# Kernel tuning notes

Hardware: AMD Instinct MI355X
Metric: run time of the kernel (lower is better)

Reference implementation:

```python
import math
import jax, jax.numpy as jnp
import numpy as np

B, CH, PN, PS = 8, 19, 128, 200
RES, SKIP, NB, S4C = 256, 256, 6, 4
L = CH * PN            # 2432, flattened (channel, patch) length
H2 = 2 * RES           # 512, S4 / attention width


def _conv1d(x, w, b, pad):
    y = jax.lax.conv_general_dilated(x, w, (1,), [(pad, pad)], dimension_numbers=('NCH', 'OIH', 'NCH'))
    return y + b[None, :, None]


def _conv2d(x, w, b, stride, pad, groups=1):
    y = jax.lax.conv_general_dilated(x, w, stride, pad, dimension_numbers=('NCHW', 'OIHW', 'NCHW'), feature_group_count=groups)
    return y + b[None, :, None, None]


def _gn(x, w, b, groups=5, eps=1e-5):
    b_, c, hh, ww = x.shape
    xg = x.reshape(b_, groups, c // groups, hh, ww)
    m = xg.mean((2, 3, 4), keepdims=True)
    v = xg.var((2, 3, 4), keepdims=True)
    xg = (xg - m) / jnp.sqrt(v + eps)
    return xg.reshape(b_, c, hh, ww) * w[None, :, None, None] + b[None, :, None, None]


def _rms(x, scale, eps=1e-8):
    # RMSNorm over channel dim (dim=1), matching source exactly
    rms = jnp.linalg.norm(x, axis=1, keepdims=True) / jnp.sqrt(jnp.asarray(x.shape[1], x.dtype))
    return scale[None, :, None] * x / (rms + eps)


def _gelu(x):
    return jax.nn.gelu(x, approximate=False)


def _forward(x, pe_w, pe_b, pi0_w, pi0_b, gn0_w, gn0_b, pi1_w, pi1_b, gn1_w, gn1_b, pi2_w, pi2_b, gn2_w, gn2_b, spec_w, spec_b, ic_w, ic_b, blk_sn, blk_cw, blk_cb, blk_k, blk_D, blk_ow, blk_ob, blk_Wv, blk_bv, blk_Wo, blk_bo, blk_rw, blk_rb, blk_sw, blk_sb, fc_w, fc_b, zc_w, zc_b, ln_w, ln_b):
    # ---------------- PatchEmbedding ----------------
    mx = x.reshape(B, 1, CH * PN, PS)
    p = _conv2d(mx, pi0_w, pi0_b, (1, 25), [(0, 0), (24, 24)])          # (B,25,CH*PN,8)
    p = _gelu(_gn(p, gn0_w, gn0_b))
    p = _gelu(_gn(_conv2d(p, pi1_w, pi1_b, (1, 1), [(0, 0), (1, 1)]), gn1_w, gn1_b))
    p = _gelu(_gn(_conv2d(p, pi2_w, pi2_b, (1, 1), [(0, 0), (1, 1)]), gn2_w, gn2_b))
    pe = jnp.transpose(p, (0, 2, 1, 3)).reshape(B, CH, PN, PS)
    spec = jnp.abs(jnp.fft.rfft(x, norm='forward'))                       # (B,CH,PN,101)
    pe = pe + jnp.einsum('bcnf,pf->bcnp', spec, spec_w) + spec_b
    pos = _conv2d(jnp.transpose(pe, (0, 3, 1, 2)), pe_w, pe_b, (1, 1), [(9, 9), (3, 3)], groups=PS)
    pe = pe + jnp.transpose(pos, (0, 2, 3, 1))
    # ---------------- b c s p -> b p (c s) ----------------
    h = jnp.transpose(pe, (0, 3, 1, 2)).reshape(B, PS, L)
    noise = jax.nn.relu(_conv1d(h, ic_w, ic_b, 0))                        # (B,RES,L)
    # ---------------- Residual group ----------------
    sk = jnp.zeros((B, SKIP, L), noise.dtype)
    hx = noise
    for i in range(NB):
        hn = _rms(hx, blk_sn[i])
        u = _gelu(_conv1d(hx + noise, blk_cw[i], blk_cb[i], 1))           # (B,H2,L)
        # S4 GConv: FFT long convolution + D skip + GLU output linear
        n = 2 * L
        uf = jnp.fft.rfft(u, n=n)                                          # (B,H2,n/2+1)
        kf = jnp.fft.rfft(blk_k[i], n=n)                                   # (S4C,H2,n/2+1)
        y = jnp.fft.irfft(uf[:, None] * kf[None], n=n)[..., :L]           # (B,S4C,H2,L)
        y = y + u[:, None] * blk_D[i][None, :, :, None]
        y = y.reshape(B, S4C * H2, L)
        y = jnp.einsum('bcl,oc->bol', y, blk_ow[i]) + blk_ob[i][None, :, None]
        h_t = y[:, :H2] * jax.nn.sigmoid(y[:, H2:])                        # GLU -> (B,H2,L)
        # window_size=1 local attention degenerates to out_proj(v_proj(x))
        v = jnp.einsum('bcl,vc->bvl', h_t, blk_Wv[i]) + blk_bv[i][None, :, None]
        a = jnp.einsum('bvl,ov->bol', v, blk_Wo[i]) + blk_bo[i][None, :, None]
        g = h_t + a
        out = jnp.tanh(g[:, :RES]) * jax.nn.sigmoid(g[:, RES:])
        hx = (hn + _conv1d(out, blk_rw[i], blk_rb[i], 0)) * math.sqrt(0.5)
        sk = sk + _conv1d(out, blk_sw[i], blk_sb[i], 0)
    sk = sk * math.sqrt(1.0 / NB)
    # ---------------- final conv + norm ----------------
    o = jax.nn.relu(_conv1d(sk, fc_w, fc_b, 0))
    o = _conv1d(o, zc_w, zc_b, 0)                                          # (B,PS,L)
    o = jnp.transpose(o.reshape(B, PS, CH, PN), (0, 2, 3, 1))              # (B,CH,PN,PS)
    m = o.mean(-1, keepdims=True)
    var = o.var(-1, keepdims=True)
    return (o - m) / jnp.sqrt(var + 1e-5) * ln_w + ln_b


def setup_inputs():
    key = jax.random.key(0)
    keys = iter(jax.random.split(key, 40))
    def rn(shape, s=0.02):
        return jax.random.normal(next(keys), shape, jnp.float32) * s
    d = {}
    d['x'] = jax.random.normal(next(keys), (B, CH, PN, PS), jnp.float32)
    d['pe_w'] = rn((PS, 1, 19, 7)); d['pe_b'] = jnp.zeros((PS,), jnp.float32)
    d['pi0_w'] = rn((25, 1, 1, 49)); d['pi0_b'] = jnp.zeros((25,), jnp.float32)
    d['gn0_w'] = jnp.ones((25,), jnp.float32); d['gn0_b'] = jnp.zeros((25,), jnp.float32)
    d['pi1_w'] = rn((25, 25, 1, 3)); d['pi1_b'] = jnp.zeros((25,), jnp.float32)
    d['gn1_w'] = jnp.ones((25,), jnp.float32); d['gn1_b'] = jnp.zeros((25,), jnp.float32)
    d['pi2_w'] = rn((25, 25, 1, 3)); d['pi2_b'] = jnp.zeros((25,), jnp.float32)
    d['gn2_w'] = jnp.ones((25,), jnp.float32); d['gn2_b'] = jnp.zeros((25,), jnp.float32)
    d['spec_w'] = rn((PS, 101)); d['spec_b'] = jnp.zeros((PS,), jnp.float32)
    d['ic_w'] = rn((RES, PS, 1)); d['ic_b'] = jnp.zeros((RES,), jnp.float32)
    d['blk_sn'] = jnp.ones((NB, RES), jnp.float32)
    d['blk_cw'] = rn((NB, H2, RES, 3)); d['blk_cb'] = jnp.zeros((NB, H2), jnp.float32)
    d['blk_k'] = rn((NB, S4C, H2, L), 0.005); d['blk_D'] = rn((NB, S4C, H2), 0.1)
    d['blk_ow'] = rn((NB, 2 * H2, S4C * H2)); d['blk_ob'] = jnp.zeros((NB, 2 * H2), jnp.float32)
    d['blk_Wv'] = rn((NB, H2, H2)); d['blk_bv'] = jnp.zeros((NB, H2), jnp.float32)
    d['blk_Wo'] = rn((NB, H2, H2)); d['blk_bo'] = jnp.zeros((NB, H2), jnp.float32)
    d['blk_rw'] = rn((NB, RES, RES, 1)); d['blk_rb'] = jnp.zeros((NB, RES), jnp.float32)
    d['blk_sw'] = rn((NB, SKIP, RES, 1)); d['blk_sb'] = jnp.zeros((NB, SKIP), jnp.float32)
    d['fc_w'] = rn((SKIP, SKIP, 1)); d['fc_b'] = jnp.zeros((SKIP,), jnp.float32)
    d['zc_w'] = rn((PS, SKIP, 1)); d['zc_b'] = jnp.zeros((PS,), jnp.float32)
    d['ln_w'] = jnp.ones((PS,), jnp.float32); d['ln_b'] = jnp.zeros((PS,), jnp.float32)
    return d


def reference(x, pe_w, pe_b, pi0_w, pi0_b, gn0_w, gn0_b, pi1_w, pi1_b, gn1_w, gn1_b, pi2_w, pi2_b, gn2_w, gn2_b, spec_w, spec_b, ic_w, ic_b, blk_sn, blk_cw, blk_cb, blk_k, blk_D, blk_ow, blk_ob, blk_Wv, blk_bv, blk_Wo, blk_bo, blk_rw, blk_rb, blk_sw, blk_sb, fc_w, fc_b, zc_w, zc_b, ln_w, ln_b):
    return _forward(x, pe_w, pe_b, pi0_w, pi0_b, gn0_w, gn0_b, pi1_w, pi1_b, gn1_w, gn1_b, pi2_w, pi2_b, gn2_w, gn2_b, spec_w, spec_b, ic_w, ic_b, blk_sn, blk_cw, blk_cb, blk_k, blk_D, blk_ow, blk_ob, blk_Wv, blk_bv, blk_Wo, blk_bo, blk_rw, blk_rb, blk_sw, blk_sb, fc_w, fc_b, zc_w, zc_b, ln_w, ln_b)
```

## Files before the change

kernel.cpp:

```cpp
#include <hip/hip_runtime.h>
#include <hip/hip_bf16.h>
#include <math.h>

#define LSEQ 2432

typedef short bf16x8 __attribute__((ext_vector_type(8)));
typedef float f32x4 __attribute__((ext_vector_type(4)));
typedef unsigned int u32;

__device__ __forceinline__ float gelu_f(float x){
  return 0.5f * x * (1.0f + erff(x * 0.70710678118654752440f));
}
__device__ __forceinline__ float sigmoid_f(float x){
  return 1.0f / (1.0f + __expf(-x));
}
__device__ __forceinline__ unsigned short f2bf(float f){
  __hip_bfloat16 h = __float2bfloat16(f);
  return *reinterpret_cast<unsigned short*>(&h);
}
__device__ __forceinline__ float bfu2f(unsigned short s){
  union { u32 u; float f; } X; X.u = ((u32)s) << 16; return X.f;
}
__device__ __forceinline__ u32 packsplit(float v){
  unsigned short hi = f2bf(v);
  float lo = v - bfu2f(hi);
  unsigned short ls = f2bf(lo);
  return (u32)hi | ((u32)ls << 16);
}

__global__ __launch_bounds__(256) void k_pi0(const float* __restrict__ x,
    const float* __restrict__ w, const float* __restrict__ bias,
    float* __restrict__ out){
  int idx = blockIdx.x * 256 + threadIdx.x;
  int o = blockIdx.y, b = blockIdx.z;
  int r = idx >> 3, wv = idx & 7;
  const float* xr = x + ((size_t)b * 2432 + r) * 200;
  const float* wt = w + o * 49;
  float acc = bias[o];
  int start = wv * 25 - 24;
  #pragma unroll
  for (int t = 0; t < 49; ++t){
    int ix = start + t;
    if (ix >= 0 && ix < 200) acc += xr[ix] * wt[t];
  }
  out[(((size_t)b * 25 + o) * 2432 + r) * 8 + wv] = acc;
}

__global__ __launch_bounds__(256) void k_gn_reduce(const float* __restrict__ p, float* __restrict__ stats){
  int b = blockIdx.x / 5, g = blockIdx.x % 5;
  const float* base = p + ((size_t)b * 25 + g * 5) * 19456;
  float s = 0.f, s2 = 0.f;
  for (int i = threadIdx.x; i < 97280; i += 256){ float v = base[i]; s += v; s2 += v * v; }
  __shared__ float sh[256], sh2[256];
  int t = threadIdx.x;
  sh[t] = s; sh2[t] = s2; __syncthreads();
  for (int off = 128; off > 0; off >>= 1){
    if (t < off){ sh[t] += sh[t+off]; sh2[t] += sh2[t+off]; }
    __syncthreads();
  }
  if (t == 0){
    float m = sh[0] / 97280.f;
    float var = sh2[0] / 97280.f - m * m;
    stats[blockIdx.x * 2] = m;
    stats[blockIdx.x * 2 + 1] = rsqrtf(var + 1e-5f);
  }
}

__global__ __launch_bounds__(256) void k_gn_apply(float* __restrict__ p, const float* __restrict__ stats,
    const float* __restrict__ gw, const float* __restrict__ gb){
  size_t i = (size_t)blockIdx.x * 256 + threadIdx.x;
  int c = (int)((i / 19456) % 25);
  int b = (int)(i / 486400);
  int g = c / 5;
  float m = stats[(b*5+g)*2], istd = stats[(b*5+g)*2+1];
  float v = (p[i] - m) * istd * gw[c] + gb[c];
  p[i] = gelu_f(v);
}

__global__ __launch_bounds__(256) void k_pconv3(const float* __restrict__ pin,
    const float* __restrict__ w, const float* __restrict__ bias, float* __restrict__ pout){
  int idx = blockIdx.x * 256 + threadIdx.x;
  int o = blockIdx.y, b = blockIdx.z;
  int r = idx >> 3, wv = idx & 7;
  const float* ib = pin + (size_t)b * 25 * 19456 + r * 8 + wv;
  const float* wo = w + o * 75;
  float acc = bias[o];
  #pragma unroll
  for (int i = 0; i < 25; ++i){
    const float* row = ib + (size_t)i * 19456;
    float w0 = wo[i*3], w1 = wo[i*3+1], w2 = wo[i*3+2];
    if (wv > 0) acc += row[-1] * w0;
    acc += row[0] * w1;
    if (wv < 7) acc += row[1] * w2;
  }
  pout[(((size_t)b*25 + o) * 2432 + r) * 8 + wv] = acc;
}

__global__ __launch_bounds__(256) void k_pe_build(const float* __restrict__ p2, float* __restrict__ pe){
  size_t i = (size_t)blockIdx.x * 256 + threadIdx.x;
  int p = (int)(i % 200);
  size_t rem = i / 200;
  int l = (int)(rem % 2432);
  int b = (int)(rem / 2432);
  pe[i] = p2[(((size_t)b*25 + (p>>3)) * 2432 + l) * 8 + (p & 7)];
}

__global__ __launch_bounds__(256) void k_spec(const float* __restrict__ x, float* __restrict__ spec){
  __shared__ float xr[200], ct[200], st[200];
  int row = blockIdx.x;
  int t = threadIdx.x;
  if (t < 200){
    xr[t] = x[(size_t)row * 200 + t];
    float ang = -0.031415926535897932385f * t;
    ct[t] = cosf(ang); st[t] = sinf(ang);
  }
  __syncthreads();
  if (t < 101){
    float re = 0.f, im = 0.f;
    int ph = 0;
    for (int k = 0; k < 200; ++k){
      re += xr[k] * ct[ph];
      im += xr[k] * st[ph];
      ph += t; if (ph >= 200) ph -= 200;
    }
    spec[(size_t)row * 101 + t] = sqrtf(re*re + im*im) * 0.005f;
  }
}

__global__ __launch_bounds__(256) void k_spec_mm(const float* __restrict__ spec,
    const float* __restrict__ sw, const float* __restrict__ sb, float* __restrict__ pe){
  __shared__ float sr[101];
  int row = blockIdx.x;
  int t = threadIdx.x;
  if (t < 101) sr[t] = spec[(size_t)row * 101 + t];
  __syncthreads();
  if (t < 200){
    const float* wr = sw + t * 101;
    float acc = sb[t];
    for (int f = 0; f < 101; ++f) acc += sr[f] * wr[f];
    pe[(size_t)row * 200 + t] += acc;
  }
}

__global__ __launch_bounds__(256) void k_trp(const float* __restrict__ pe, float* __restrict__ peT){
  __shared__ float ts[32][33];
  int l0 = blockIdx.x * 32, c0 = blockIdx.y * 32, b = blockIdx.z;
  int t = threadIdx.x;
  int i = t >> 5, j = t & 31;
  #pragma unroll
  for (int pass = 0; pass < 4; ++pass){
    int ii = i + pass * 8;
    int c = c0 + j;
    ts[ii][j] = (c < 200) ? pe[((size_t)b * 2432 + l0 + ii) * 200 + c] : 0.f;
  }
  __syncthreads();
  #pragma unroll
  for (int pass = 0; pass < 4; ++pass){
    int ii = i + pass * 8;
    int c = c0 + ii;
    if (c < 200) peT[((size_t)b * 200 + c) * 2432 + l0 + j] = ts[j][ii];
  }
}

__global__ __launch_bounds__(128) void k_hbuild2(const float* __restrict__ peT,
    const float* __restrict__ pw, const float* __restrict__ pb, float* __restrict__ h){
  __shared__ float T[19][136];
  __shared__ float wsh[133];
  int c = blockIdx.x, p = blockIdx.y, b = blockIdx.z;
  int tid = threadIdx.x;
  const float* pr = peT + ((size_t)b * 200 + p) * 2432;
  for (int e = tid; e < 19 * 136; e += 128){
    int a = e / 136, m = e % 136;
    int hh = c - 9 + a, ww = m - 3;
    float v = 0.f;
    if (hh >= 0 && hh < 19 && ww >= 0 && ww < 128) v = pr[hh * 128 + ww];
    T[a][m] = v;
  }
  for (int e = tid; e < 133; e += 128) wsh[e] = pw[p * 133 + e];
  __syncthreads();
  int j = tid;
  float conv = pb[p];
  #pragma unroll
  for (int a = 0; a < 19; ++a){
    #pragma unroll
    for (int tt = 0; tt < 7; ++tt) conv += T[a][j + tt] * wsh[a * 7 + tt];
  }
  float orig = T[9][j + 3];
  h[((size_t)b * 200 + p) * 2432 + c * 128 + j] = orig + conv;
}

__global__ __launch_bounds__(256) void k_wcast(const float* __restrict__ src,
    unsigned short* __restrict__ dst, int O, int Kin, int Kpad){
  size_t i = (size_t)blockIdx.x * 256 + threadIdx.x;
  if (i >= (size_t)O * Kpad) return;
  int k = (int)(i % Kpad);
  int o = (int)(i / Kpad);
  dst[i] = (k < Kin) ? f2bf(src[(size_t)o * Kin + k]) : 0;
}

__global__ __launch_bounds__(256) void k_wcast_glu(const float* __restrict__ src,
    unsigned short* __restrict__ dst){
  size_t i = (size_t)blockIdx.x * 256 + threadIdx.x;
  if (i >= (size_t)6 * 1024 * 2048) return;
  int k = (int)(i % 2048);
  size_t rem = i / 2048;
  int ro = (int)(rem % 1024);
  int blk = (int)(rem / 1024);
  int j = (ro >> 1) + (ro & 1) * 512;
  dst[i] = f2bf(src[((size_t)blk * 1024 + j) * 2048 + k]);
}

__global__ __launch_bounds__(256) void k_castT(const float* __restrict__ in,
    unsigned short* __restrict__ out, int C, int Kpad, int cbase){
  __shared__ float ts[32][33];
  int l0 = blockIdx.x * 32, c0 = blockIdx.y * 32, b = blockIdx.z;
  int t = threadIdx.x;
  int i = t >> 5, j = t & 31;
  #pragma unroll
  for (int pass = 0; pass < 4; ++pass){
    int ci = c0 + i + pass * 8;
    ts[i + pass * 8][j] = (ci < C) ? in[((size_t)b * C + ci) * LSEQ + l0 + j] : 0.f;
  }
  __syncthreads();
  #pragma unroll
  for (int pass = 0; pass < 4; ++pass){
    int li = l0 + i + pass * 8;
    out[((size_t)b * LSEQ + li) * Kpad + cbase + c0 + j] = f2bf(ts[j][i + pass * 8]);
  }
}

__global__ __launch_bounds__(256) void k_packT(const float* __restrict__ A,
    const float* __restrict__ N, u32* __restrict__ out){
  __shared__ float ts[32][33];
  int l0 = blockIdx.x * 32, c0 = blockIdx.y * 32, b = blockIdx.z;
  int t = threadIdx.x;
  int i = t >> 5, j = t & 31;
  #pragma unroll
  for (int pass = 0; pass < 4; ++pass){
    int ci = c0 + i + pass * 8;
    size_t ii = ((size_t)b * 256 + ci) * LSEQ + l0 + j;
    ts[i + pass * 8][j] = A[ii] + N[ii];
  }
  __syncthreads();
  #pragma unroll
  for (int pass = 0; pass < 4; ++pass){
    int li = l0 + i + pass * 8;
    out[((size_t)b * LSEQ + li) * 256 + c0 + j] = packsplit(ts[j][i + pass * 8]);
  }
}

__global__ __launch_bounds__(256) void k_wpack3(const float* __restrict__ cw, u32* __restrict__ Wp){
  int i = blockIdx.x * 256 + threadIdx.x;
  int o = i / 768, rem = i % 768;
  int t = rem / 256, c = rem % 256;
  Wp[i] = packsplit(cw[((size_t)o * 256 + c) * 3 + t]);
}

__global__ __launch_bounds__(256) void k_gateT(const float* __restrict__ ht,
    const float* __restrict__ a, unsigned short* __restrict__ out){
  __shared__ float ts[32][33];
  int l0 = blockIdx.x * 32, c0 = blockIdx.y * 32, b = blockIdx.z;
  int t = threadIdx.x;
  int i = t >> 5, j = t & 31;
  #pragma unroll
  for (int pass = 0; pass < 4; ++pass){
    int ci = c0 + i + pass * 8;
    size_t i1 = ((size_t)b * 512 + ci) * LSEQ + l0 + j;
    size_t i2 = ((size_t)b * 512 + ci + 256) * LSEQ + l0 + j;
    float g1 = ht[i1] + a[i1];
    float g2 = ht[i2] + a[i2];
    ts[i + pass * 8][j] = tanhf(g1) * sigmoid_f(g2);
  }
  __syncthreads();
  #pragma unroll
  for (int pass = 0; pass < 4; ++pass){
    int li = l0 + i + pass * 8;
    out[((size_t)b * LSEQ + li) * 256 + c0 + j] = f2bf(ts[j][i + pass * 8]);
  }
}

__global__ __launch_bounds__(256) void k_rmsr(const float* __restrict__ hx, float* __restrict__ rinv){
  int idx = blockIdx.x * 256 + threadIdx.x;
  int b = idx / 2432, l = idx % 2432;
  const float* p = hx + (size_t)b * 256 * LSEQ + l;
  float s = 0.f;
  #pragma unroll 8
  for (int c = 0; c < 256; ++c){ float v = p[(size_t)c * LSEQ]; s += v * v; }
  rinv[idx] = 1.0f / (sqrtf(s * (1.0f/256.0f)) + 1e-8f);
}

__global__ __launch_bounds__(256) void k_bgemm(const unsigned short* __restrict__ Wb,
    const unsigned short* __restrict__ Xb, const float* __restrict__ bias,
    const float* __restrict__ res, const float* __restrict__ sn,
    const float* __restrict__ rinv, float* __restrict__ out,
    int O, int Kpad, float alpha, float fs, int act, int accf){
  __shared__ unsigned short Ws[128 * 40];
  __shared__ unsigned short Xs[128 * 40];
  int l0 = blockIdx.x * 128, o0 = blockIdx.y * 128, b = blockIdx.z;
  int tid = threadIdx.x;
  int w = tid >> 6, lane = tid & 63;
  int ow_ = (w & 1) * 64, lw_ = (w >> 1) * 64;
  int m = lane & 15, q = (lane >> 4) & 3;
  const unsigned short* Xbb = Xb + (size_t)b * 2432 * Kpad;
  f32x4 acc[4][4] = {};
  for (int k0 = 0; k0 < Kpad; k0 += 32){
    #pragma unroll
    for (int r = 0; r < 2; ++r){
      int idx = tid + r * 256;
      int row = idx >> 2, cq = (idx & 3) * 8;
      uint4 v = make_uint4(0u, 0u, 0u, 0u);
      int o = o0 + row;
      if (o < O) v = *(const uint4*)(Wb + (size_t)o * Kpad + k0 + cq);
      *(uint4*)&Ws[row * 40 + cq] = v;
      uint4 xv = *(const uint4*)(Xbb + (size_t)(l0 + row) * Kpad + k0 + cq);
      *(uint4*)&Xs[row * 40 + cq] = xv;
    }
    __syncthreads();
    bf16x8 A[4], Bf[4];
    #pragma unroll
    for (int t = 0; t < 4; ++t) A[t] = *(const bf16x8*)&Ws[(ow_ + t * 16 + m) * 40 + q * 8];
    #pragma unroll
    for (int u = 0; u < 4; ++u) Bf[u] = *(const bf16x8*)&Xs[(lw_ + u * 16 + m) * 40 + q * 8];
    #pragma unroll
    for (int t = 0; t < 4; ++t)
      #pragma unroll
      for (int u = 0; u < 4; ++u)
        acc[t][u] = __builtin_amdgcn_mfma_f32_16x16x32_bf16(A[t], Bf[u], acc[t][u], 0, 0, 0);
    __syncthreads();
  }
  if (act == 3){
    #pragma unroll
    for (int t = 0; t < 4; ++t){
      #pragma unroll
      for (int u = 0; u < 4; ++u){
        int l = l0 + lw_ + u * 16 + m;
        #pragma unroll
        for (int r = 0; r < 4; r += 2){
          int ro = o0 + ow_ + t * 16 + q * 4 + r;
          int j = ro >> 1;
          float v1 = acc[t][u][r]   + bias[j];
          float v2 = acc[t][u][r+1] + bias[j + 512];
          out[((size_t)b * 512 + j) * LSEQ + l] = v1 * sigmoid_f(v2);
        }
      }
    }
    return;
  }
  #pragma unroll
  for (int t = 0; t < 4; ++t){
    #pragma unroll
    for (int u = 0; u < 4; ++u){
      int l = l0 + lw_ + u * 16 + m;
      #pragma unroll
      for (int r = 0; r < 4; ++r){
        int o = o0 + ow_ + t * 16 + q * 4 + r;
        if (o >= O) continue;
        size_t oi = ((size_t)b * O + o) * LSEQ + l;
        float v = alpha * acc[t][u][r];
        if (bias) v += bias[o];
        if (res){
          if (sn) v += sn[o] * res[oi] * rinv[b * 2432 + l];
          else v += res[oi];
        }
        if (accf) v += out[oi];
        if (act == 1) v = fmaxf(v, 0.f);
        out[oi] = v * fs;
      }
    }
  }
}

__device__ __forceinline__ bf16x8 s4_mk(u32 a, u32 b, u32 c, u32 d){
  union { u32 u[4]; bf16x8 v; } X; X.u[0]=a; X.u[1]=b; X.u[2]=c; X.u[3]=d; return X.v;
}
#define S4_P16H(a,b) __builtin_amdgcn_perm((a),(b),0x05040100u)
#define S4_P16L(a,b) __builtin_amdgcn_perm((a),(b),0x07060302u)

__global__ __launch_bounds__(256) void k_conv3m(const u32* __restrict__ Wp,
    const float* __restrict__ bias, const u32* __restrict__ Xp, float* __restrict__ U){
  __shared__ u32 Ws[128 * 36];
  __shared__ u32 Xs[128 * 36];
  int l0 = blockIdx.x * 128, o0 = blockIdx.y * 128, b = blockIdx.z;
  int tid = threadIdx.x;
  int w = tid >> 6, lane = tid & 63;
  int ow_ = (w & 1) * 64, lw_ = (w >> 1) * 64;
  int m = lane & 15, q = (lane >> 4) & 3;
  const u32* Xb = Xp + (size_t)b * 2432 * 256;
  f32x4 acc[4][4] = {};
  for (int s = 0; s < 24; ++s){
    int t = s >> 3, k0 = (s & 7) << 5;
    #pragma unroll
    for (int r = 0; r < 4; ++r){
      int idx = tid + r * 256;
      int row = idx >> 3, cq = (idx & 7) * 4;
      *(uint4*)&Ws[row * 36 + cq] = *(const uint4*)(Wp + (size_t)(o0 + row) * 768 + t * 256 + k0 + cq);
      int li = l0 + row + t - 1;
      uint4 xv = make_uint4(0u, 0u, 0u, 0u);
      if (li >= 0 && li < 2432) xv = *(const uint4*)(Xb + (size_t)li * 256 + k0 + cq);
      *(uint4*)&Xs[row * 36 + cq] = xv;
    }
    __syncthreads();
    bf16x8 Ah[4], Al[4], Bh[4], Bl[4];
    #pragma unroll
    for (int tt = 0; tt < 4; ++tt){
      const u32* p = &Ws[(ow_ + tt * 16 + m) * 36 + q * 8];
      u32 w0=p[0],w1=p[1],w2=p[2],w3=p[3],w4=p[4],w5=p[5],w6=p[6],w7=p[7];
      Ah[tt] = s4_mk(S4_P16H(w1,w0), S4_P16H(w3,w2), S4_P16H(w5,w4), S4_P16H(w7,w6));
      Al[tt] = s4_mk(S4_P16L(w1,w0), S4_P16L(w3,w2), S4_P16L(w5,w4), S4_P16L(w7,w6));
    }
    #pragma unroll
    for (int uu = 0; uu < 4; ++uu){
      const u32* p = &Xs[(lw_ + uu * 16 + m) * 36 + q * 8];
      u32 w0=p[0],w1=p[1],w2=p[2],w3=p[3],w4=p[4],w5=p[5],w6=p[6],w7=p[7];
      Bh[uu] = s4_mk(S4_P16H(w1,w0), S4_P16H(w3,w2), S4_P16H(w5,w4), S4_P16H(w7,w6));
      Bl[uu] = s4_mk(S4_P16L(w1,w0), S4_P16L(w3,w2), S4_P16L(w5,w4), S4_P16L(w7,w6));
    }
    #pragma unroll
    for (int tt = 0; tt < 4; ++tt)
      #pragma unroll
      for (int uu = 0; uu < 4; ++uu){
        acc[tt][uu] = __builtin_amdgcn_mfma_f32_16x16x32_bf16(Ah[tt], Bh[uu], acc[tt][uu], 0, 0, 0);
        acc[tt][uu] = __builtin_amdgcn_mfma_f32_16x16x32_bf16(Al[tt], Bh[uu], acc[tt][uu], 0, 0, 0);
        acc[tt][uu] = __builtin_amdgcn_mfma_f32_16x16x32_bf16(Ah[tt], Bl[uu], acc[tt][uu], 0, 0, 0);
      }
    __syncthreads();
  }
  #pragma unroll
  for (int tt = 0; tt < 4; ++tt){
    #pragma unroll
    for (int uu = 0; uu < 4; ++uu){
      int l = l0 + lw_ + uu * 16 + m;
      #pragma unroll
      for (int r = 0; r < 4; ++r){
        int o = o0 + ow_ + tt * 16 + q * 4 + r;
        U[((size_t)b * 512 + o) * LSEQ + l] = gelu_f(acc[tt][uu][r] + bias[o]);
      }
    }
  }
}

#define S4_SU 2464
#define S4_UPLANE (8*S4_SU*2)
#define S4_ULO  S4_UPLANE
#define S4_REV  (2*S4_UPLANE)
#define S4_TS   (S4_REV + 2856*4)
#define S4_LDSZ (S4_TS + 4*576)

#define S4_FILL(SL) { \
  int Wc = Wp > 0 ? Wp : 0; \
  int ib = rl + Wc; \
  u32 w0=RV[ib], w1=RV[ib+1], w2=RV[ib+2], w3=RV[ib+3], w4=RV[ib+4], w5=RV[ib+5], w6=RV[ib+6], w7=RV[ib+7]; \
  Ph[SL] = s4_mk(S4_P16H(w1,w0), S4_P16H(w3,w2), S4_P16H(w5,w4), S4_P16H(w7,w6)); \
  Pl[SL] = s4_mk(S4_P16L(w1,w0), S4_P16L(w3,w2), S4_P16L(w5,w4), S4_P16L(w7,w6)); \
  Wp -= 32; }

#define S4_MM(ph,d,BH,BL) \
  acc[d] = __builtin_amdgcn_mfma_f32_16x16x32_bf16(Ph[((ph)+5+(d))%12], BH, acc[d], 0, 0, 0); \
  acc[d] = __builtin_amdgcn_mfma_f32_16x16x32_bf16(Pl[((ph)+5+(d))%12], BH, acc[d], 0, 0, 0); \
  acc[d] = __builtin_amdgcn_mfma_f32_16x16x32_bf16(Ph[((ph)+5+(d))%12], BL, acc[d], 0, 0, 0);

#define S4_PHASE(ph,BC,BN) { \
  S4_FILL(((ph)+4)%12); \
  int bn = j0 - 32; bn = bn > 2400 ? 2400 : bn; bn = bn < 0 ? 2432 : bn; \
  const char* bp = LB + ubo + 2*bn; \
  Bh##BN = *(const bf16x8*)bp; \
  Bl##BN = *(const bf16x8*)(bp + S4_ULO); \
  S4_MM(ph,0,Bh##BC,Bl##BC) S4_MM(ph,1,Bh##BC,Bl##BC) S4_MM(ph,2,Bh##BC,Bl##BC) S4_MM(ph,3,Bh##BC,Bl##BC) \
  S4_MM(ph,4,Bh##BC,Bl##BC) S4_MM(ph,5,Bh##BC,Bl##BC) S4_MM(ph,6,Bh##BC,Bl##BC) S4_MM(ph,7,Bh##BC,Bl##BC) \
  j0 -= 32; }

__global__ __launch_bounds__(256, 1) void k_s4m(const float* __restrict__ ksrc,
    const float* __restrict__ Dv, const float* __restrict__ u, float* __restrict__ y){
  extern __shared__ char LB[];
  ushort* UH = (ushort*)LB;
  ushort* UL = (ushort*)(LB + S4_ULO);
  u32* RV = (u32*)(LB + S4_REV);
  int h = blockIdx.x;
  int tid = threadIdx.x;
  for (int e = tid; e < 8 * 608; e += 256){
    int b = e / 608, c4 = e % 608;
    float4 v = *(const float4*)(u + ((size_t)b * 512 + h) * 2432 + c4 * 4);
    u32 p0 = packsplit(v.x), p1 = packsplit(v.y), p2 = packsplit(v.z), p3 = packsplit(v.w);
    uint2 hw, lw;
    hw.x = (p0 & 0xffffu) | (p1 << 16);
    hw.y = (p2 & 0xffffu) | (p3 << 16);
    lw.x = (p0 >> 16) | (p1 & 0xffff0000u);
    lw.y = (p2 >> 16) | (p3 & 0xffff0000u);
    *(uint2*)(LB + (size_t)b * (S4_SU*2) + c4 * 8) = hw;
    *(uint2*)(LB + S4_ULO + (size_t)b * (S4_SU*2) + c4 * 8) = lw;
  }
  if (tid < 256){
    int b = tid >> 5, i = tid & 31;
    UH[b * S4_SU + 2432 + i] = 0;
    UL[b * S4_SU + 2432 + i] = 0;
  }
  {
    const float* kg = ksrc + (size_t)h * 2432;
    for (int e = tid; e < 2856; e += 256){
      u32 v = 0;
      int t = 2704 - e;
      if (t >= 0 && t < 2432) v = packsplit(kg[t]);
      RV[e] = v;
    }
  }
  __syncthreads();

  int lane = tid & 63;
  int wid = __builtin_amdgcn_readfirstlane(tid >> 6);
  int m = lane & 15, qq = lane >> 4;
  int rl = 16 - m + 8 * qq;
  int ubo = (m & 7) * (S4_SU*2) + qq * 16;
  float dv = Dv[h];
  float* TSp = (float*)(LB + S4_TS + wid * 576);
  static const int GT[2][5] = {{9,6,4,2,0},{8,7,5,3,1}};

  #pragma unroll 1
  for (int c = 0; c < 5; ++c){
    int g = GT[wid >> 1][c];
    int Lb = 256 * g + ((wid & 1) << 4);
    int ltop = Lb + 224;
    int J0 = ((ltop + 15) >> 5) << 5;
    int W0 = 2688 - ltop + J0;
    int NS = (J0 >> 5) + 1;
    int nIt = (NS + 11) / 12;

    f32x4 acc[8];
    bf16x8 Ph[12], Pl[12];
    bf16x8 Bh0, Bl0, Bh1, Bl1;
    {
      f32x4 za = {0.f, 0.f, 0.f, 0.f};
      acc[0]=za; acc[1]=za; acc[2]=za; acc[3]=za; acc[4]=za; acc[5]=za; acc[6]=za; acc[7]=za;
      bf16x8 zz = s4_mk(0u,0u,0u,0u);
      Ph[5]=zz; Ph[6]=zz; Ph[7]=zz; Ph[8]=zz; Ph[9]=zz; Ph[10]=zz; Ph[11]=zz; Ph[4]=zz;
      Pl[5]=zz; Pl[6]=zz; Pl[7]=zz; Pl[8]=zz; Pl[9]=zz; Pl[10]=zz; Pl[11]=zz; Pl[4]=zz;
    }
    int Wp = W0;
    S4_FILL(0) S4_FILL(1) S4_FILL(2) S4_FILL(3)
    int j0 = J0;
    {
      int bj0 = j0 > 2400 ? 2400 : j0;
      const char* bp0 = LB + ubo + 2 * bj0;
      Bh0 = *(const bf16x8*)bp0;
      Bl0 = *(const bf16x8*)(bp0 + S4_ULO);
    }
    #pragma unroll 1
    for (int it = 0; it < nIt; ++it){
      S4_PHASE(0,0,1) S4_PHASE(1,1,0) S4_PHASE(2,0,1) S4_PHASE(3,1,0)
      S4_PHASE(4,0,1) S4_PHASE(5,1,0) S4_PHASE(6,0,1) S4_PHASE(7,1,0)
      S4_PHASE(8,0,1) S4_PHASE(9,1,0) S4_PHASE(10,0,1) S4_PHASE(11,1,0)
    }
    #pragma unroll
    for (int d = 0; d < 8; ++d){
      int ld = Lb + 32 * d;
      if (ld < 2432){
        if (m < 8){
          TSp[(qq*4+0)*9 + m] = acc[d][0];
          TSp[(qq*4+1)*9 + m] = acc[d][1];
          TSp[(qq*4+2)*9 + m] = acc[d][2];
          TSp[(qq*4+3)*9 + m] = acc[d][3];
        }
        __builtin_amdgcn_wave_barrier();
        #pragma unroll
        for (int p = 0; p < 2; ++p){
          int li = lane & 15, bb = (lane >> 4) + 4 * p;
          float v = TSp[li*9 + bb];
          int l = ld + li;
          float uv = bfu2f(UH[bb * S4_SU + l]) + bfu2f(UL[bb * S4_SU + l]);
          y[((size_t)bb * 512 + h) * 2432 + l] = v + dv * uv;
        }
        __builtin_amdgcn_wave_barrier();
      }
    }
  }
}

__global__ __launch_bounds__(256) void k_ln(const float* __restrict__ o2,
    const float* __restrict__ lw, const float* __restrict__ lb2, float* __restrict__ out){
  __shared__ float s1[256], s2[256];
  int row = blockIdx.x;
  int b = row / 2432, l = row % 2432;
  int t = threadIdx.x;
  float v = 0.f;
  if (t < 200) v = o2[((size_t)b * 200 + t) * LSEQ + l];
  s1[t] = v; s2[t] = v * v;
  __syncthreads();
  for (int off = 128; off > 0; off >>= 1){
    if (t < off){ s1[t] += s1[t + off]; s2[t] += s2[t + off]; }
    __syncthreads();
  }
  float m = s1[0] * 0.005f;
  float var = s2[0] * 0.005f - m * m;
  float istd = rsqrtf(var + 1e-5f);
  if (t < 200) out[(size_t)row * 200 + t] = (v - m) * istd * lw[t] + lb2[t];
}

extern "C" void kernel_launch(void* const* d_in, const int* in_sizes, int n_in,
                              void* d_out, int out_size, void* d_ws, size_t ws_size,
                              hipStream_t stream){
  const float* x     = (const float*)d_in[0];
  const float* pe_w  = (const float*)d_in[1];
  const float* pe_b  = (const float*)d_in[2];
  const float* pi0_w = (const float*)d_in[3];
  const float* pi0_b = (const float*)d_in[4];
  const float* gn0_w = (const float*)d_in[5];
  const float* gn0_b = (const float*)d_in[6];
  const float* pi1_w = (const float*)d_in[7];
  const float* pi1_b = (const float*)d_in[8];
  const float* gn1_w = (const float*)d_in[9];
  const float* gn1_b = (const float*)d_in[10];
  const float* pi2_w = (const float*)d_in[11];
  const float* pi2_b = (const float*)d_in[12];
  const float* gn2_w = (const float*)d_in[13];
  const float* gn2_b = (const float*)d_in[14];
  const float* spec_w= (const float*)d_in[15];
  const float* spec_b= (const float*)d_in[16];
  const float* ic_w  = (const float*)d_in[17];
  const float* ic_b  = (const float*)d_in[18];
  const float* blk_sn= (const float*)d_in[19];
  const float* blk_cw= (const float*)d_in[20];
  const float* blk_cb= (const float*)d_in[21];
  const float* blk_k = (const float*)d_in[22];
  const float* blk_D = (const float*)d_in[23];
  const float* blk_ow= (const float*)d_in[24];
  const float* blk_ob= (const float*)d_in[25];
  const float* blk_Wv= (const float*)d_in[26];
  const float* blk_bv= (const float*)d_in[27];
  const float* blk_Wo= (const float*)d_in[28];
  const float* blk_bo= (const float*)d_in[29];
  const float* blk_rw= (const float*)d_in[30];
  const float* blk_rb= (const float*)d_in[31];
  const float* blk_sw= (const float*)d_in[32];
  const float* blk_sb= (const float*)d_in[33];
  const float* fc_w  = (const float*)d_in[34];
  const float* fc_b  = (const float*)d_in[35];
  const float* zc_w  = (const float*)d_in[36];
  const float* zc_b  = (const float*)d_in[37];
  const float* ln_w  = (const float*)d_in[38];
  const float* ln_b  = (const float*)d_in[39];

  static int s4m_attr = 0;
  if (!s4m_attr){
    hipFuncSetAttribute(reinterpret_cast<const void*>(k_s4m),
                        hipFuncAttributeMaxDynamicSharedMemorySize, S4_LDSZ);
    s4m_attr = 1;
  }

  float* Wsp = (float*)d_ws;
  const size_t NLL = (size_t)8 * 256 * 2432;
  float* noise = Wsp;
  float* hxb   = Wsp + NLL;
  float* skb   = Wsp + 2 * NLL;
  float* ub    = Wsp + 3 * NLL;
  float* ysb   = Wsp + 5 * NLL;
  float* htb   = ysb;
  unsigned short* actT = (unsigned short*)(Wsp + 7 * NLL);
  unsigned short* wB = (unsigned short*)(Wsp + 11 * NLL);
  unsigned short* owB = wB;
  unsigned short* WvB = wB + 12582912;
  unsigned short* WoB = wB + 14155776;
  unsigned short* rwB = wB + 15728640;
  unsigned short* swB = wB + 16121856;
  unsigned short* icB = wB + 16515072;
  unsigned short* fcB = wB + 16572416;
  unsigned short* zcB = wB + 16637952;
  float* rinv   = Wsp + 11 * NLL + 8344576;
  float* gnstats= rinv + 19456;
  u32* WpB = (u32*)(Wsp + 63152208);
  u32* XpT = (u32*)(Wsp + 7 * NLL);

  float* p0 = ub;
  float* p1 = ysb;
  float* p2 = ub;
  float* pe = Wsp + 7 * NLL;
  float* spec = Wsp + 8 * NLL;
  float* peT = skb;
  float* hb = hxb;

  const float SQ05 = 0.70710678118654752440f;
  const float SQ16 = 0.40824829046386301637f;

  k_wcast_glu<<<49152,256,0,stream>>>(blk_ow, owB);
  k_wcast<<<(3072*512+255)/256,256,0,stream>>>(blk_Wv, WvB, 3072, 512, 512);
  k_wcast<<<(3072*512+255)/256,256,0,stream>>>(blk_Wo, WoB, 3072, 512, 512);
  k_wcast<<<(1536*256+255)/256,256,0,stream>>>(blk_rw, rwB, 1536, 256, 256);
  k_wcast<<<(1536*256+255)/256,256,0,stream>>>(blk_sw, swB, 1536, 256, 256);
  k_wcast<<<(256*224+255)/256,256,0,stream>>>(ic_w, icB, 256, 200, 224);
  k_wcast<<<(256*256+255)/256,256,0,stream>>>(fc_w, fcB, 256, 256, 256);
  k_wcast<<<(200*256+255)/256,256,0,stream>>>(zc_w, zcB, 200, 256, 256);

  k_pi0<<<dim3(76,25,8), 256, 0, stream>>>(x, pi0_w, pi0_b, p0);
  k_gn_reduce<<<40,256,0,stream>>>(p0, gnstats);
  k_gn_apply<<<15200,256,0,stream>>>(p0, gnstats, gn0_w, gn0_b);
  k_pconv3<<<dim3(76,25,8),256,0,stream>>>(p0, pi1_w, pi1_b, p1);
  k_gn_reduce<<<40,256,0,stream>>>(p1, gnstats);
  k_gn_apply<<<15200,256,0,stream>>>(p1, gnstats, gn1_w, gn1_b);
  k_pconv3<<<dim3(76,25,8),256,0,stream>>>(p1, pi2_w, pi2_b, p2);
  k_gn_reduce<<<40,256,0,stream>>>(p2, gnstats);
  k_gn_apply<<<15200,256,0,stream>>>(p2, gnstats, gn2_w, gn2_b);
  k_pe_build<<<15200,256,0,stream>>>(p2, pe);
  k_spec<<<19456,256,0,stream>>>(x, spec);
  k_spec_mm<<<19456,256,0,stream>>>(spec, spec_w, spec_b, pe);
  k_trp<<<dim3(76,7,8),256,0,stream>>>(pe, peT);
  k_hbuild2<<<dim3(19,200,8),128,0,stream>>>(peT, pe_w, pe_b, hb);
  k_castT<<<dim3(76,7,8),256,0,stream>>>(hb, actT, 200, 224, 0);
  k_bgemm<<<dim3(19,2,8),256,0,stream>>>(icB, actT, ic_b, nullptr, nullptr, nullptr,
                                         noise, 256, 224, 1.f, 1.f, 1, 0);
  hipMemcpyAsync(hxb, noise, NLL * sizeof(float), hipMemcpyDeviceToDevice, stream);

  for (int i = 0; i < 6; ++i){
    const float* sn = blk_sn + i * 256;
    const float* cw = blk_cw + (size_t)i * 512 * 768;
    const float* cb = blk_cb + i * 512;
    const float* ob = blk_ob + i * 1024;
    const float* bv = blk_bv + i * 512;
    const float* bo = blk_bo + i * 512;
    const float* rb = blk_rb + i * 256;
    const float* sb = blk_sb + i * 256;

    k_rmsr<<<76,256,0,stream>>>(hxb, rinv);
    k_packT<<<dim3(76,8,8),256,0,stream>>>(hxb, noise, XpT);
    k_wpack3<<<1536,256,0,stream>>>(cw, WpB);
    k_conv3m<<<dim3(19,4,8),256,0,stream>>>(WpB, cb, XpT, ub);
    for (int s = 0; s < 4; ++s){
      const float* kw = blk_k + ((size_t)i * 4 + s) * 512 * 2432;
      const float* Dvp = blk_D + ((size_t)i * 4 + s) * 512;
      k_s4m<<<dim3(512),256,S4_LDSZ,stream>>>(kw, Dvp, ub, ysb);
      k_castT<<<dim3(76,16,8),256,0,stream>>>(ysb, actT, 512, 2048, s * 512);
    }
    k_bgemm<<<dim3(19,8,8),256,0,stream>>>(owB + (size_t)i*1024*2048, actT, ob,
                                           nullptr, nullptr, nullptr, htb,
                                           1024, 2048, 1.f, 1.f, 3, 0);
    k_castT<<<dim3(76,16,8),256,0,stream>>>(htb, actT, 512, 512, 0);
    k_bgemm<<<dim3(19,4,8),256,0,stream>>>(WvB + (size_t)i*512*512, actT, bv,
                                           nullptr, nullptr, nullptr, ub,
                                           512, 512, 1.f, 1.f, 0, 0);
    k_castT<<<dim3(76,16,8),256,0,stream>>>(ub, actT, 512, 512, 0);
    k_bgemm<<<dim3(19,4,8),256,0,stream>>>(WoB + (size_t)i*512*512, actT, bo,
                                           nullptr, nullptr, nullptr, ub,
                                           512, 512, 1.f, 1.f, 0, 0);
    k_gateT<<<dim3(76,8,8),256,0,stream>>>(htb, ub, actT);
    k_bgemm<<<dim3(19,2,8),256,0,stream>>>(rwB + (size_t)i*256*256, actT, rb,
                                           hxb, sn, rinv, hxb,
                                           256, 256, 1.f, SQ05, 0, 0);
    k_bgemm<<<dim3(19,2,8),256,0,stream>>>(swB + (size_t)i*256*256, actT, sb,
                                           nullptr, nullptr, nullptr, skb,
                                           256, 256, 1.f, 1.f, 0, i==0?0:1);
  }

  k_castT<<<dim3(76,8,8),256,0,stream>>>(skb, actT, 256, 256, 0);
  k_bgemm<<<dim3(19,2,8),256,0,stream>>>(fcB, actT, fc_b, nullptr, nullptr, nullptr,
                                         ub, 256, 256, SQ16, 1.f, 1, 0);
  k_castT<<<dim3(76,8,8),256,0,stream>>>(ub, actT, 256, 256, 0);
  k_bgemm<<<dim3(19,2,8),256,0,stream>>>(zcB, actT, zc_b, nullptr, nullptr, nullptr,
                                         ysb, 200, 256, 1.f, 1.f, 0, 0);
  k_ln<<<19456,256,0,stream>>>(ysb, ln_w, ln_b, (float*)d_out);
}
```

Baseline: 9.410 ms.

## Widen S4 kernel to 8 waves with rebalanced chunk schedule; tile patch convs in LDS

The S4 long-convolution kernel now runs 512 threads (8 waves) per head instead of 256. A new per-wave chunk table spreads the 20 causal half-chunks across waves to balance the triangular workload, and the per-wave scratch region in LDS grows to match. The patch-embedding conv kernels (pi0 and the 3-tap pconv) now stage input rows and weights in shared memory and compute all 25 output channels per thread, which removes redundant global reads across the output-channel grid dimension. Risks are more LDS and register pressure in k_s4m and higher register use in the conv kernels, which hold 49 or 75 values per thread.

```diff
diff --git a/kernel.cpp b/kernel.cpp
--- a/kernel.cpp
+++ b/kernel.cpp
@@ -28,22 +28,36 @@
   return (u32)hi | ((u32)ls << 16);
 }
 
-__global__ __launch_bounds__(256) void k_pi0(const float* __restrict__ x,
+__global__ __launch_bounds__(256) void k_pi0b(const float* __restrict__ x,
     const float* __restrict__ w, const float* __restrict__ bias,
     float* __restrict__ out){
-  int idx = blockIdx.x * 256 + threadIdx.x;
-  int o = blockIdx.y, b = blockIdx.z;
-  int r = idx >> 3, wv = idx & 7;
-  const float* xr = x + ((size_t)b * 2432 + r) * 200;
-  const float* wt = w + o * 49;
-  float acc = bias[o];
+  __shared__ float xs[32][200];
+  __shared__ float ws[25][49];
+  __shared__ float bs[25];
+  int r0 = blockIdx.x * 32, b = blockIdx.y;
+  int tid = threadIdx.x;
+  const float* xb = x + ((size_t)b * 2432 + r0) * 200;
+  for (int e = tid; e < 1600; e += 256){
+    int row = e / 50, c4 = e % 50;
+    *(float4*)&xs[row][c4 * 4] = *(const float4*)(xb + row * 200 + c4 * 4);
+  }
+  for (int e = tid; e < 1225; e += 256) ws[e / 49][e % 49] = w[e];
+  if (tid < 25) bs[tid] = bias[tid];
+  __syncthreads();
+  int row = tid >> 3, wv = tid & 7;
   int start = wv * 25 - 24;
+  float tap[49];
   #pragma unroll
   for (int t = 0; t < 49; ++t){
     int ix = start + t;
-    if (ix >= 0 && ix < 200) acc += xr[ix] * wt[t];
-  }
-  out[(((size_t)b * 25 + o) * 2432 + r) * 8 + wv] = acc;
+    tap[t] = (ix >= 0 && ix < 200) ? xs[row][ix] : 0.f;
+  }
+  for (int o = 0; o < 25; ++o){
+    float acc = bs[o];
+    #pragma unroll
+    for (int t = 0; t < 49; ++t) acc += tap[t] * ws[o][t];
+    out[(((size_t)b * 25 + o) * 2432 + (r0 + row)) * 8 + wv] = acc;
+  }
 }
 
 __global__ __launch_bounds__(256) void k_gn_reduce(const float* __restrict__ p, float* __restrict__ stats){
@@ -77,23 +91,36 @@
   p[i] = gelu_f(v);
 }
 
-__global__ __launch_bounds__(256) void k_pconv3(const float* __restrict__ pin,
+__global__ __launch_bounds__(256) void k_pconv3b(const float* __restrict__ pin,
     const float* __restrict__ w, const float* __restrict__ bias, float* __restrict__ pout){
-  int idx = blockIdx.x * 256 + threadIdx.x;
-  int o = blockIdx.y, b = blockIdx.z;
-  int r = idx >> 3, wv = idx & 7;
-  const float* ib = pin + (size_t)b * 25 * 19456 + r * 8 + wv;
-  const float* wo = w + o * 75;
-  float acc = bias[o];
+  __shared__ float T[25][256];
+  __shared__ float ws[25][75];
+  __shared__ float bs[25];
+  int r0 = blockIdx.x * 32, b = blockIdx.y;
+  int tid = threadIdx.x;
+  const float* pb = pin + (size_t)b * 25 * 19456 + r0 * 8;
+  for (int e = tid; e < 25 * 64; e += 256){
+    int i = e / 64, c4 = e % 64;
+    *(float4*)&T[i][c4 * 4] = *(const float4*)(pb + (size_t)i * 19456 + c4 * 4);
+  }
+  for (int e = tid; e < 1875; e += 256) ws[e / 75][e % 75] = w[e];
+  if (tid < 25) bs[tid] = bias[tid];
+  __syncthreads();
+  int wv = tid & 7;
+  float xm[25], x0[25], xp[25];
   #pragma unroll
   for (int i = 0; i < 25; ++i){
-    const float* row = ib + (size_t)i * 19456;
-    float w0 = wo[i*3], w1 = wo[i*3+1], w2 = wo[i*3+2];
-    if (wv > 0) acc += row[-1] * w0;
-    acc += row[0] * w1;
-    if (wv < 7) acc += row[1] * w2;
-  }
-  pout[(((size_t)b*25 + o) * 2432 + r) * 8 + wv] = acc;
+    x0[i] = T[i][tid];
+    xm[i] = (wv > 0) ? T[i][tid - 1] : 0.f;
+    xp[i] = (wv < 7) ? T[i][tid + 1] : 0.f;
+  }
+  for (int o = 0; o < 25; ++o){
+    float acc = bs[o];
+    #pragma unroll
+    for (int i = 0; i < 25; ++i)
+      acc += xm[i] * ws[o][i*3] + x0[i] * ws[o][i*3+1] + xp[i] * ws[o][i*3+2];
+    pout[(((size_t)b * 25 + o) * 2432 + r0) * 8 + tid] = acc;
+  }
 }
 
 __global__ __launch_bounds__(256) void k_pe_build(const float* __restrict__ p2, float* __restrict__ pe){
@@ -444,7 +471,7 @@
 #define S4_ULO  S4_UPLANE
 #define S4_REV  (2*S4_UPLANE)
 #define S4_TS   (S4_REV + 2856*4)
-#define S4_LDSZ (S4_TS + 4*576)
+#define S4_LDSZ (S4_TS + 8*576*4)
 
 #define S4_FILL(SL) { \
   int Wc = Wp > 0 ? Wp : 0; \
@@ -469,7 +496,7 @@
   S4_MM(ph,4,Bh##BC,Bl##BC) S4_MM(ph,5,Bh##BC,Bl##BC) S4_MM(ph,6,Bh##BC,Bl##BC) S4_MM(ph,7,Bh##BC,Bl##BC) \
   j0 -= 32; }
 
-__global__ __launch_bounds__(256, 1) void k_s4m(const float* __restrict__ ksrc,
+__global__ __launch_bounds__(512, 1) void k_s4m(const float* __restrict__ ksrc,
     const float* __restrict__ Dv, const float* __restrict__ u, float* __restrict__ y){
   extern __shared__ char LB[];
   ushort* UH = (ushort*)LB;
@@ -477,7 +504,7 @@
   u32* RV = (u32*)(LB + S4_REV);
   int h = blockIdx.x;
   int tid = threadIdx.x;
-  for (int e = tid; e < 8 * 608; e += 256){
+  for (int e = tid; e < 8 * 608; e += 512){
     int b = e / 608, c4 = e % 608;
     float4 v = *(const float4*)(u + ((size_t)b * 512 + h) * 2432 + c4 * 4);
     u32 p0 = packsplit(v.x), p1 = packsplit(v.y), p2 = packsplit(v.z), p3 = packsplit(v.w);
@@ -496,7 +523,7 @@
   }
   {
     const float* kg = ksrc + (size_t)h * 2432;
-    for (int e = tid; e < 2856; e += 256){
+    for (int e = tid; e < 2856; e += 512){
       u32 v = 0;
       int t = 2704 - e;
       if (t >= 0 && t < 2432) v = packsplit(kg[t]);
@@ -511,13 +538,17 @@
   int rl = 16 - m + 8 * qq;
   int ubo = (m & 7) * (S4_SU*2) + qq * 16;
   float dv = Dv[h];
-  float* TSp = (float*)(LB + S4_TS + wid * 576);
-  static const int GT[2][5] = {{9,6,4,2,0},{8,7,5,3,1}};
+  float* TSp = (float*)(LB + S4_TS + wid * 2304);
+  static const signed char GC[8][5] = {
+    {19,10,-1,-1,-1},{18,12,-1,-1,-1},{17, 8,-1,-1,-1},{15, 7,-1,-1,-1},
+    {16,11,-1,-1,-1},{14, 9,-1,-1,-1},{13, 6, 4,-1,-1},{ 5, 3, 2, 1, 0}};
 
   #pragma unroll 1
   for (int c = 0; c < 5; ++c){
-    int g = GT[wid >> 1][c];
-    int Lb = 256 * g + ((wid & 1) << 4);
+    int gc = GC[wid][c];
+    if (gc < 0) break;
+    int g = gc >> 1, half = gc & 1;
+    int Lb = 256 * g + (half << 4);
     int ltop = Lb + 224;
     int J0 = ((ltop + 15) >> 5) << 5;
     int W0 = 2688 - ltop + J0;
@@ -688,13 +719,13 @@
   k_wcast<<<(256*256+255)/256,256,0,stream>>>(fc_w, fcB, 256, 256, 256);
   k_wcast<<<(200*256+255)/256,256,0,stream>>>(zc_w, zcB, 200, 256, 256);
 
-  k_pi0<<<dim3(76,25,8), 256, 0, stream>>>(x, pi0_w, pi0_b, p0);
+  k_pi0b<<<dim3(76,8), 256, 0, stream>>>(x, pi0_w, pi0_b, p0);
   k_gn_reduce<<<40,256,0,stream>>>(p0, gnstats);
   k_gn_apply<<<15200,256,0,stream>>>(p0, gnstats, gn0_w, gn0_b);
-  k_pconv3<<<dim3(76,25,8),256,0,stream>>>(p0, pi1_w, pi1_b, p1);
+  k_pconv3b<<<dim3(76,8),256,0,stream>>>(p0, pi1_w, pi1_b, p1);
   k_gn_reduce<<<40,256,0,stream>>>(p1, gnstats);
   k_gn_apply<<<15200,256,0,stream>>>(p1, gnstats, gn1_w, gn1_b);
-  k_pconv3<<<dim3(76,25,8),256,0,stream>>>(p1, pi2_w, pi2_b, p2);
+  k_pconv3b<<<dim3(76,8),256,0,stream>>>(p1, pi2_w, pi2_b, p2);
   k_gn_reduce<<<40,256,0,stream>>>(p2, gnstats);
   k_gn_apply<<<15200,256,0,stream>>>(p2, gnstats, gn2_w, gn2_b);
   k_pe_build<<<15200,256,0,stream>>>(p2, pe);
@@ -724,7 +755,7 @@
     for (int s = 0; s < 4; ++s){
       const float* kw = blk_k + ((size_t)i * 4 + s) * 512 * 2432;
       const float* Dvp = blk_D + ((size_t)i * 4 + s) * 512;
-      k_s4m<<<dim3(512),256,S4_LDSZ,stream>>>(kw, Dvp, ub, ysb);
+      k_s4m<<<dim3(512),512,S4_LDSZ,stream>>>(kw, Dvp, ub, ysb);
       k_castT<<<dim3(76,16,8),256,0,stream>>>(ysb, actT, 512, 2048, s * 512);
     }
     k_bgemm<<<dim3(19,8,8),256,0,stream>>>(owB + (size_t)i*1024*2048, actT, ob,
```

After: 8.430 ms. 10.4% less time.
